# Performance work log

Hardware: AMD Instinct MI355X
Metric: run time of the kernel (lower is better)

Reference implementation:

```python
import jax, jax.numpy as jnp
import numpy as np
from jax import lax

DIM = 256
PROJ = 128
NPOS = 8          # ceil(log2(2*64+5))
EXT = 64          # attnExtension
NLAYERS = 4
HEADS = 4
KDIM = PROJ + NPOS
EPS = 1e-5


def _ln(x):
    # LayerNorm over last dim, no affine (elementwise_affine=False)
    mu = jnp.mean(x, axis=-1, keepdims=True)
    var = jnp.mean(jnp.square(x - mu), axis=-1, keepdims=True)
    return (x - mu) * lax.rsqrt(var + EPS)


def setup_inputs() -> dict:
    key = jax.random.key(0)
    ks = jax.random.split(key, 18)
    L = 2048
    s = 0.05
    return {
        "input": jax.random.normal(ks[0], (L, PROJ), jnp.float32),
        "residual": jax.random.normal(ks[1], (5 * L, DIM), jnp.float32),
        "W_proj": jax.random.normal(ks[2], (5 * DIM, KDIM), jnp.float32) * s,
        "b_proj": jnp.zeros((5 * DIM,), jnp.float32),
        "Wq": jax.random.normal(ks[3], (DIM, DIM), jnp.float32) * s,
        "bq": jnp.zeros((DIM,), jnp.float32),
        "Wk": jax.random.normal(ks[4], (DIM, KDIM), jnp.float32) * s,
        "bk": jnp.zeros((DIM,), jnp.float32),
        "Wv": jax.random.normal(ks[5], (DIM, KDIM), jnp.float32) * s,
        "bv": jnp.zeros((DIM,), jnp.float32),
        "Wo": jax.random.normal(ks[6], (DIM, DIM), jnp.float32) * s,
        "bo": jnp.zeros((DIM,), jnp.float32),
        "conv_w": jax.random.normal(ks[7], (NLAYERS, DIM, DIM, 3), jnp.float32) * s,
        "conv_b": jnp.zeros((NLAYERS, DIM), jnp.float32),
        "W_skip": jax.random.normal(ks[8], (DIM, DIM), jnp.float32) * s,
        "b_skip": jnp.zeros((DIM,), jnp.float32),
    }


def reference(input, residual, W_proj, b_proj, Wq, bq, Wk, bk, Wv, bv,
              Wo, bo, conv_w, conv_b, W_skip, b_skip):
    L = input.shape[0]
    T = 5 * L  # tgt length
    hd = DIM // HEADS

    # positional embeddings: pos[:, i] = (arange(L) % 2^(i+1)) / 2^i
    n = jnp.arange(L, dtype=input.dtype)[:, None]
    i = jnp.arange(NPOS, dtype=input.dtype)[None, :]
    pos = jnp.mod(n, 2.0 ** (i + 1.0)) / (2.0 ** i)

    src = jnp.concatenate([input, pos], axis=1)            # (L, KDIM)
    tgt = (src @ W_proj.T + b_proj).reshape(T, DIM)        # (5L, DIM)

    # banded mask: row j may attend col i iff 5i-EXT <= j < 5i+5+EXT
    j = jnp.arange(T)[:, None]
    ii = jnp.arange(L)[None, :]
    d = j - 5 * ii
    allowed = (d >= -EXT) & (d < 5 + EXT)                  # (5L, L)

    # multihead attention (eval mode, dropout skipped)
    q = (tgt @ Wq.T + bq).reshape(T, HEADS, hd).transpose(1, 0, 2)
    k = (src @ Wk.T + bk).reshape(L, HEADS, hd).transpose(1, 0, 2)
    v = (src @ Wv.T + bv).reshape(L, HEADS, hd).transpose(1, 0, 2)
    scores = jnp.einsum('hqd,hkd->hqk', q, k) / jnp.sqrt(jnp.asarray(hd, q.dtype))
    scores = jnp.where(allowed[None], scores, -jnp.inf)
    attn = jax.nn.softmax(scores, axis=-1)
    ctx = jnp.einsum('hqk,hkd->hqd', attn, v).transpose(1, 0, 2).reshape(T, DIM)
    attn_out = ctx @ Wo.T + bo

    cnn_in = _ln(attn_out) + residual                      # (5L, DIM)

    # spectral-norm conv stack (weights assumed pre-normalized) + tanh
    x = cnn_in.T[None]                                     # (1, DIM, 5L)
    for l in range(NLAYERS):
        x = jnp.tanh(
            lax.conv_general_dilated(x, conv_w[l], window_strides=(1,),
                                     padding=[(1, 1)])
            + conv_b[l][None, :, None])
    cnn_out = x[0].T                                       # (5L, DIM)

    return _ln(cnn_out + cnn_in @ W_skip.T + b_skip)
```

## Files before the change

### kernel.cpp

```cpp
#include <hip/hip_runtime.h>
#include <hip/hip_bf16.h>

#define PROJ 128
#define KPAD 192
#define EPS 1e-5f

typedef __attribute__((ext_vector_type(4))) float f32x4;
typedef __attribute__((ext_vector_type(8))) short bf16x8;
typedef __attribute__((ext_vector_type(4))) unsigned int u32x4;

__device__ inline float bflo(unsigned u){ union{unsigned x;float f;}c; c.x = u<<16; return c.f; }
__device__ inline float bfhi(unsigned u){ union{unsigned x;float f;}c; c.x = u & 0xffff0000u; return c.f; }
__device__ inline float bf2f(unsigned short u){ union{unsigned x;float f;}c; c.x = ((unsigned)u)<<16; return c.f; }
__device__ inline unsigned short f2bf(float f){
    union{float f; unsigned u;} c; c.f = f;
    unsigned r = c.u + 0x7fff + ((c.u >> 16) & 1);
    return (unsigned short)(r >> 16);
}

__global__ __launch_bounds__(256) void prep_all(
    const float* __restrict__ W_proj, const float* __restrict__ Wq,
    const float* __restrict__ Wk, const float* __restrict__ Wv,
    const float* __restrict__ Wo, const float* __restrict__ Ws,
    const float* __restrict__ convw, const float* __restrict__ input,
    unsigned short* __restrict__ Wpb, unsigned short* __restrict__ Wqb,
    unsigned short* __restrict__ Wkb, unsigned short* __restrict__ Wvb,
    unsigned short* __restrict__ Wob, unsigned short* __restrict__ Wsb,
    unsigned short* __restrict__ Wcb, unsigned short* __restrict__ srcb,
    unsigned short* __restrict__ cinp, int L, int T)
{
    int idx = blockIdx.x * 256 + threadIdx.x;
    if (idx < 245760) {
        int r = idx / 192, c = idx % 192;
        Wpb[idx] = (c < 136) ? f2bf(W_proj[(size_t)r * 136 + c]) : (unsigned short)0;
        return;
    }
    idx -= 245760;
    if (idx < 65536) { Wqb[idx] = f2bf(Wq[idx]); return; }
    idx -= 65536;
    if (idx < 49152) {
        int r = idx / 192, c = idx % 192;
        Wkb[idx] = (c < 136) ? f2bf(Wk[(size_t)r * 136 + c]) : (unsigned short)0;
        return;
    }
    idx -= 49152;
    if (idx < 49152) {
        int r = idx / 192, c = idx % 192;
        Wvb[idx] = (c < 136) ? f2bf(Wv[(size_t)r * 136 + c]) : (unsigned short)0;
        return;
    }
    idx -= 49152;
    if (idx < 65536) { Wob[idx] = f2bf(Wo[idx]); return; }
    idx -= 65536;
    if (idx < 65536) {
        int e = idx & 7;
        int lane = (idx >> 3) & 63;
        int fr = (idx >> 9) & 3;
        int wid = (idx >> 11) & 7;
        int kt = idx >> 14;
        int j = fr >> 1, ks = fr & 1;
        int kq = lane >> 4, rowf = lane & 15;
        int o = wid * 32 + j * 16 + rowf;
        int c = kt * 64 + ks * 32 + kq * 8 + e;
        Wsb[idx] = f2bf(Ws[(size_t)o * 256 + c]);
        return;
    }
    idx -= 65536;
    if (idx < 786432) {
        int e = idx & 7;
        int lane = (idx >> 3) & 63;
        int fr = (idx >> 9) & 3;
        int wid = (idx >> 11) & 7;
        int ktl = idx >> 14;
        int l = ktl / 12, kt = ktl % 12;
        int j = fr >> 1, ks = fr & 1;
        int kq = lane >> 4, rowf = lane & 15;
        int o = wid * 32 + j * 16 + rowf;
        int c = kt * 64 + ks * 32 + kq * 8 + e;
        int ktap = c >> 8, ci = c & 255;
        Wcb[idx] = f2bf(convw[(((size_t)l * 256 + o) * 256 + ci) * 3 + ktap]);
        return;
    }
    idx -= 786432;
    if (idx < L * KPAD) {
        int n = idx / KPAD, c = idx % KPAD;
        float v = 0.f;
        if (c < PROJ) v = input[(size_t)n * PROJ + c];
        else if (c < PROJ + 8) {
            int i = c - PROJ;
            int mask = (2 << i) - 1;
            v = (float)(n & mask) / (float)(1 << i);
        }
        srcb[idx] = f2bf(v);
        return;
    }
    idx -= L * KPAD;
    if (idx < 512) {
        int row = idx >> 8, c = idx & 255;
        size_t o = (row == 0) ? (size_t)c : (size_t)(T + 1) * 256 + c;
        cinp[o] = 0;
    }
}

__device__ __forceinline__ void gemm_core_64x128(
    unsigned short (&As)[64][72], unsigned short (&Bs)[128][72],
    const unsigned short* __restrict__ A, int lda,
    const unsigned short* __restrict__ B, int ldb,
    const float* __restrict__ bias,
    unsigned short* __restrict__ C, int ldc,
    int K, int m0, int n0)
{
    const int tid = threadIdx.x;
    const int lane = tid & 63;
    const int wid = tid >> 6;
    const int wm = wid >> 1, wn = wid & 1;

    const int ar = tid >> 2, asg = tid & 3;
    const int br = tid >> 1, bsg = tid & 1;

    const unsigned short* Ap = A + (size_t)(m0 + ar) * lda + asg * 16;
    const unsigned short* Bp = B + (size_t)(n0 + br) * ldb + bsg * 32;

    u32x4 ra0, ra1, rb0, rb1, rb2, rb3;
    auto loadregs = [&](int k0) {
        ra0 = *(const u32x4*)(Ap + k0);
        ra1 = *(const u32x4*)(Ap + k0 + 8);
        rb0 = *(const u32x4*)(Bp + k0);
        rb1 = *(const u32x4*)(Bp + k0 + 8);
        rb2 = *(const u32x4*)(Bp + k0 + 16);
        rb3 = *(const u32x4*)(Bp + k0 + 24);
    };
    auto stlds = [&]() {
        *(u32x4*)&As[ar][asg * 16]      = ra0;
        *(u32x4*)&As[ar][asg * 16 + 8]  = ra1;
        *(u32x4*)&Bs[br][bsg * 32]      = rb0;
        *(u32x4*)&Bs[br][bsg * 32 + 8]  = rb1;
        *(u32x4*)&Bs[br][bsg * 32 + 16] = rb2;
        *(u32x4*)&Bs[br][bsg * 32 + 24] = rb3;
    };

    f32x4 acc[2][4];
    #pragma unroll
    for (int i = 0; i < 2; ++i)
        #pragma unroll
        for (int j = 0; j < 4; ++j) acc[i][j] = (f32x4){0.f, 0.f, 0.f, 0.f};

    loadregs(0);
    stlds();
    __syncthreads();

    const int rowf = lane & 15, kb = lane >> 4;
    const int ktiles = K >> 6;
    for (int kt = 0; kt < ktiles; ++kt) {
        if (kt + 1 < ktiles) loadregs((kt + 1) << 6);
        #pragma unroll
        for (int ks = 0; ks < 2; ++ks) {
            bf16x8 af[2], bfr[4];
            #pragma unroll
            for (int i = 0; i < 2; ++i)
                af[i] = *(const bf16x8*)&As[wm * 32 + i * 16 + rowf][ks * 32 + kb * 8];
            #pragma unroll
            for (int j = 0; j < 4; ++j)
                bfr[j] = *(const bf16x8*)&Bs[wn * 64 + j * 16 + rowf][ks * 32 + kb * 8];
            #pragma unroll
            for (int i = 0; i < 2; ++i)
                #pragma unroll
                for (int j = 0; j < 4; ++j)
                    acc[i][j] = __builtin_amdgcn_mfma_f32_16x16x32_bf16(af[i], bfr[j], acc[i][j], 0, 0, 0);
        }
        __syncthreads();
        if (kt + 1 < ktiles) { stlds(); __syncthreads(); }
    }

    const int rq = lane >> 4;
    #pragma unroll
    for (int i = 0; i < 2; ++i) {
        int gm = m0 + wm * 32 + i * 16 + rq * 4;
        #pragma unroll
        for (int j = 0; j < 4; ++j) {
            int gn = n0 + wn * 64 + j * 16 + rowf;
            float bv = bias[gn];
            #pragma unroll
            for (int r = 0; r < 4; ++r)
                C[(size_t)(gm + r) * ldc + gn] = f2bf(acc[i][j][r] + bv);
        }
    }
}

__global__ __launch_bounds__(256) void gemm_proj(
    const unsigned short* __restrict__ A, int lda,
    const unsigned short* __restrict__ B, int ldb,
    const float* __restrict__ bias,
    unsigned short* __restrict__ C, int ldc, int K)
{
    __shared__ unsigned short As[64][72];
    __shared__ unsigned short Bs[128][72];
    gemm_core_64x128(As, Bs, A, lda, B, ldb, bias, C, ldc, K,
                     blockIdx.y * 64, blockIdx.x * 128);
}

__global__ __launch_bounds__(256) void qkv_fused(
    const unsigned short* __restrict__ tgt,
    const unsigned short* __restrict__ src,
    const unsigned short* __restrict__ Wqb,
    const unsigned short* __restrict__ Wkb,
    const unsigned short* __restrict__ Wvb,
    const float* __restrict__ bq, const float* __restrict__ bk,
    const float* __restrict__ bv,
    unsigned short* __restrict__ qb, unsigned short* __restrict__ kb,
    unsigned short* __restrict__ vb)
{
    __shared__ unsigned short As[64][72];
    __shared__ unsigned short Bs[128][72];
    int bi = blockIdx.x;
    const unsigned short *A, *B;
    const float* bias;
    unsigned short* C;
    int lda, ldb, K, m0, n0;
    if (bi < 320) {
        A = tgt; B = Wqb; bias = bq; C = qb; lda = 256; ldb = 256; K = 256;
        m0 = (bi >> 1) * 64; n0 = (bi & 1) * 128;
    } else if (bi < 384) {
        int t = bi - 320;
        A = src; B = Wkb; bias = bk; C = kb; lda = KPAD; ldb = 192; K = 192;
        m0 = (t >> 1) * 64; n0 = (t & 1) * 128;
    } else {
        int t = bi - 384;
        A = src; B = Wvb; bias = bv; C = vb; lda = KPAD; ldb = 192; K = 192;
        m0 = (t >> 1) * 64; n0 = (t & 1) * 128;
    }
    gemm_core_64x128(As, Bs, A, lda, B, ldb, bias, C, 256, K, m0, n0);
}

__global__ __launch_bounds__(512) void gemm_ln0(
    const unsigned short* __restrict__ A, int lda,
    const unsigned short* __restrict__ B,
    const float* __restrict__ bias,
    const float* __restrict__ residual,
    unsigned short* __restrict__ out_bf)
{
    __shared__ unsigned short As[64][72];
    __shared__ unsigned short Bs[256][72];
    __shared__ float redS[64][4];
    __shared__ float redQ[64][4];

    const int tid = threadIdx.x;
    const int lane = tid & 63;
    const int wid = tid >> 6;
    const int wm = wid >> 2, wn = wid & 3;
    const int m0 = blockIdx.x * 64;

    const int arow = tid >> 3, acol = (tid & 7) * 8;
    const int brow = tid >> 1, bcol = (tid & 1) * 32;
    const unsigned short* Ap = A + (size_t)(m0 + arow) * lda + acol;
    const unsigned short* Bp = B + (size_t)brow * 256 + bcol;

    u32x4 ra, rb0, rb1, rb2, rb3;
    auto loadregs = [&](int k0) {
        ra  = *(const u32x4*)(Ap + k0);
        rb0 = *(const u32x4*)(Bp + k0);
        rb1 = *(const u32x4*)(Bp + k0 + 8);
        rb2 = *(const u32x4*)(Bp + k0 + 16);
        rb3 = *(const u32x4*)(Bp + k0 + 24);
    };
    auto stlds = [&]() {
        *(u32x4*)&As[arow][acol]       = ra;
        *(u32x4*)&Bs[brow][bcol]       = rb0;
        *(u32x4*)&Bs[brow][bcol + 8]   = rb1;
        *(u32x4*)&Bs[brow][bcol + 16]  = rb2;
        *(u32x4*)&Bs[brow][bcol + 24]  = rb3;
    };

    f32x4 acc[2][4];
    #pragma unroll
    for (int i = 0; i < 2; ++i)
        #pragma unroll
        for (int j = 0; j < 4; ++j) acc[i][j] = (f32x4){0.f, 0.f, 0.f, 0.f};

    loadregs(0);
    stlds();
    __syncthreads();

    const int rowf = lane & 15, kb = lane >> 4;
    #pragma unroll
    for (int kt = 0; kt < 4; ++kt) {
        if (kt < 3) loadregs((kt + 1) << 6);
        #pragma unroll
        for (int ks = 0; ks < 2; ++ks) {
            bf16x8 af[2], bfr[4];
            #pragma unroll
            for (int i = 0; i < 2; ++i)
                af[i] = *(const bf16x8*)&As[wm * 32 + i * 16 + rowf][ks * 32 + kb * 8];
            #pragma unroll
            for (int j = 0; j < 4; ++j)
                bfr[j] = *(const bf16x8*)&Bs[wn * 64 + j * 16 + rowf][ks * 32 + kb * 8];
            #pragma unroll
            for (int i = 0; i < 2; ++i)
                #pragma unroll
                for (int j = 0; j < 4; ++j)
                    acc[i][j] = __builtin_amdgcn_mfma_f32_16x16x32_bf16(af[i], bfr[j], acc[i][j], 0, 0, 0);
        }
        __syncthreads();
        if (kt < 3) { stlds(); __syncthreads(); }
    }

    const int rq = lane >> 4;
    float val[2][4][4];
    #pragma unroll
    for (int i = 0; i < 2; ++i)
        #pragma unroll
        for (int j = 0; j < 4; ++j) {
            int gn = wn * 64 + j * 16 + rowf;
            float bv = bias[gn];
            #pragma unroll
            for (int r = 0; r < 4; ++r) val[i][j][r] = acc[i][j][r] + bv;
        }

    #pragma unroll
    for (int i = 0; i < 2; ++i)
        #pragma unroll
        for (int r = 0; r < 4; ++r) {
            float s = val[i][0][r] + val[i][1][r] + val[i][2][r] + val[i][3][r];
            float q = val[i][0][r] * val[i][0][r] + val[i][1][r] * val[i][1][r]
                    + val[i][2][r] * val[i][2][r] + val[i][3][r] * val[i][3][r];
            #pragma unroll
            for (int m = 1; m < 16; m <<= 1) {
                s += __shfl_xor(s, m, 64);
                q += __shfl_xor(q, m, 64);
            }
            if (rowf == 0) {
                int row = wm * 32 + i * 16 + rq * 4 + r;
                redS[row][wn] = s;
                redQ[row][wn] = q;
            }
        }
    __syncthreads();

    #pragma unroll
    for (int i = 0; i < 2; ++i) {
        #pragma unroll
        for (int r = 0; r < 4; ++r) {
            int row = wm * 32 + i * 16 + rq * 4 + r;
            int gm = m0 + row;
            float s = redS[row][0] + redS[row][1] + redS[row][2] + redS[row][3];
            float q = redQ[row][0] + redQ[row][1] + redQ[row][2] + redQ[row][3];
            float mu = s * (1.f / 256.f);
            float var = q * (1.f / 256.f) - mu * mu;
            float rs = rsqrtf(var + EPS);
            #pragma unroll
            for (int j = 0; j < 4; ++j) {
                int gn = wn * 64 + j * 16 + rowf;
                float nv = (val[i][j][r] - mu) * rs + residual[(size_t)gm * 256 + gn];
                out_bf[(size_t)(gm + 1) * 256 + gn] = f2bf(nv);
            }
        }
    }
}

__global__ __launch_bounds__(256) void attn16(
    const unsigned short* __restrict__ q,
    const unsigned short* __restrict__ k,
    const unsigned short* __restrict__ v,
    unsigned short* __restrict__ ctx, int L)
{
    __shared__ unsigned short ksm[30][264];
    __shared__ unsigned short vsm[30][264];
    const int j0 = blockIdx.x * 16;
    const int iblk0 = (j0 >= 68) ? (j0 - 64) / 5 : 0;
    int ihim = (j0 + 79) / 5; if (ihim > L - 1) ihim = L - 1;
    const int NR = ihim - iblk0 + 1;

    for (int e = threadIdx.x; e < 30 * 32; e += 256) {
        int rr = e >> 5, cc = (e & 31) * 8;
        u32x4 kz = {0, 0, 0, 0}, vz = {0, 0, 0, 0};
        if (rr < NR) {
            kz = *(const u32x4*)&k[(size_t)(iblk0 + rr) * 256 + cc];
            vz = *(const u32x4*)&v[(size_t)(iblk0 + rr) * 256 + cc];
        }
        *(u32x4*)&ksm[rr][cc] = kz;
        *(u32x4*)&vsm[rr][cc] = vz;
    }
    __syncthreads();

    const int tid = threadIdx.x;
    const int h = tid >> 6, lane = tid & 63;
    const int qq = lane & 15, p = lane >> 4;
    const int j = j0 + qq;
    const int colb = h * 64 + p * 16;

    float qr[16];
    {
        u32x4 q0 = *(const u32x4*)&q[(size_t)j * 256 + colb];
        u32x4 q1 = *(const u32x4*)&q[(size_t)j * 256 + colb + 8];
        #pragma unroll
        for (int w = 0; w < 4; ++w) {
            qr[2 * w]     = bflo(q0[w]) * 0.125f;
            qr[2 * w + 1] = bfhi(q0[w]) * 0.125f;
            qr[8 + 2 * w]     = bflo(q1[w]) * 0.125f;
            qr[8 + 2 * w + 1] = bfhi(q1[w]) * 0.125f;
        }
    }
    const int ilo = (j >= 68) ? (j - 64) / 5 : 0;
    int ihi = (j + 64) / 5; if (ihi > L - 1) ihi = L - 1;

    float sc[30];
    #pragma unroll
    for (int t = 0; t < 30; ++t) {
        int i = iblk0 + t;
        u32x4 k0 = *(const u32x4*)&ksm[t][colb];
        u32x4 k1 = *(const u32x4*)&ksm[t][colb + 8];
        float s = 0.f;
        #pragma unroll
        for (int w = 0; w < 4; ++w) {
            s += qr[2 * w]     * bflo(k0[w]);
            s += qr[2 * w + 1] * bfhi(k0[w]);
            s += qr[8 + 2 * w]     * bflo(k1[w]);
            s += qr[8 + 2 * w + 1] * bfhi(k1[w]);
        }
        s += __shfl_xor(s, 16, 64);
        s += __shfl_xor(s, 32, 64);
        sc[t] = (i >= ilo && i <= ihi) ? s : -1e30f;
    }
    float mx = -1e30f;
    #pragma unroll
    for (int t = 0; t < 30; ++t) mx = fmaxf(mx, sc[t]);
    float den = 0.f, o[16];
    #pragma unroll
    for (int d = 0; d < 16; ++d) o[d] = 0.f;
    #pragma unroll
    for (int t = 0; t < 30; ++t) {
        float pt = __expf(sc[t] - mx);
        den += pt;
        u32x4 v0 = *(const u32x4*)&vsm[t][colb];
        u32x4 v1 = *(const u32x4*)&vsm[t][colb + 8];
        #pragma unroll
        for (int w = 0; w < 4; ++w) {
            o[2 * w]     += pt * bflo(v0[w]);
            o[2 * w + 1] += pt * bfhi(v0[w]);
            o[8 + 2 * w]     += pt * bflo(v1[w]);
            o[8 + 2 * w + 1] += pt * bfhi(v1[w]);
        }
    }
    float inv = 1.f / den;
    #pragma unroll
    for (int d = 0; d < 16; ++d)
        ctx[(size_t)j * 256 + colb + d] = f2bf(o[d] * inv);
}

#define CVALID 40
template<int NKT, bool ISCONV>
__device__ __forceinline__ void frag_gemm(
    const unsigned short* __restrict__ Wp,
    unsigned short (*actin)[264],
    f32x4 (&acc)[3][2], int wid, int lane)
{
    const int rowf = lane & 15, kq = lane >> 4;
    const unsigned short* base = Wp + wid * 2048 + lane * 8;
    bf16x8 b0, b1, b2, b3, c0, c1, c2, c3, d0, d1, d2, d3;
    b0 = *(const bf16x8*)(base);
    b1 = *(const bf16x8*)(base + 512);
    b2 = *(const bf16x8*)(base + 1024);
    b3 = *(const bf16x8*)(base + 1536);
    c0 = *(const bf16x8*)(base + 16384);
    c1 = *(const bf16x8*)(base + 16384 + 512);
    c2 = *(const bf16x8*)(base + 16384 + 1024);
    c3 = *(const bf16x8*)(base + 16384 + 1536);
    d0 = b0; d1 = b1; d2 = b2; d3 = b3;
    #pragma unroll
    for (int kt = 0; kt < NKT; ++kt) {
        if (kt + 2 < NKT) {
            const unsigned short* nb = base + (kt + 2) * 16384;
            d0 = *(const bf16x8*)(nb);
            d1 = *(const bf16x8*)(nb + 512);
            d2 = *(const bf16x8*)(nb + 1024);
            d3 = *(const bf16x8*)(nb + 1536);
        }
        const int dt = ISCONV ? (kt >> 2) : 1;
        const int cb = ISCONV ? ((kt & 3) * 64) : (kt * 64);
        #pragma unroll
        for (int ks = 0; ks < 2; ++ks) {
            bf16x8 a0 = *(const bf16x8*)&actin[rowf + dt][cb + ks * 32 + kq * 8];
            bf16x8 a1 = *(const bf16x8*)&actin[16 + rowf + dt][cb + ks * 32 + kq * 8];
            bf16x8 a2 = *(const bf16x8*)&actin[32 + rowf + dt][cb + ks * 32 + kq * 8];
            bf16x8 w0 = ks ? b1 : b0;
            bf16x8 w1 = ks ? b3 : b2;
            acc[0][0] = __builtin_amdgcn_mfma_f32_16x16x32_bf16(a0, w0, acc[0][0], 0, 0, 0);
            acc[0][1] = __builtin_amdgcn_mfma_f32_16x16x32_bf16(a0, w1, acc[0][1], 0, 0, 0);
            acc[1][0] = __builtin_amdgcn_mfma_f32_16x16x32_bf16(a1, w0, acc[1][0], 0, 0, 0);
            acc[1][1] = __builtin_amdgcn_mfma_f32_16x16x32_bf16(a1, w1, acc[1][1], 0, 0, 0);
            acc[2][0] = __builtin_amdgcn_mfma_f32_16x16x32_bf16(a2, w0, acc[2][0], 0, 0, 0);
            acc[2][1] = __builtin_amdgcn_mfma_f32_16x16x32_bf16(a2, w1, acc[2][1], 0, 0, 0);
        }
        b0 = c0; b1 = c1; b2 = c2; b3 = c3;
        c0 = d0; c1 = d1; c2 = d2; c3 = d3;
    }
}

__global__ __launch_bounds__(512, 2) void conv_skip_ln(
    const unsigned short* __restrict__ cinp,
    const unsigned short* __restrict__ Wcb,
    const float* __restrict__ conv_b,
    const unsigned short* __restrict__ Wsb,
    const float* __restrict__ b_skip,
    float* __restrict__ out, int T)
{
    __shared__ unsigned short actA[50][264];
    __shared__ unsigned short actB[50][264];
    __shared__ float redS[48][8];
    __shared__ float redQ[48][8];

    const int tid = threadIdx.x;
    const int lane = tid & 63;
    const int wid = tid >> 6;
    const int rowf = lane & 15;
    const int kq = lane >> 4;
    const int t0 = blockIdx.x * CVALID;

    for (int e = tid; e < 50 * 32; e += 512) {
        int b = e >> 5, c = (e & 31) * 8;
        int g = t0 - 5 + b;
        u32x4 z = {0, 0, 0, 0};
        if (g >= -1 && g <= T)
            z = *(const u32x4*)&cinp[(size_t)(g + 1) * 256 + c];
        *(u32x4*)&actA[b][c] = z;
    }
    if (tid < 256) actB[0][tid] = 0; else actB[49][tid - 256] = 0;
    __syncthreads();

    f32x4 skipacc[3][2];
    #pragma unroll
    for (int i = 0; i < 3; ++i)
        #pragma unroll
        for (int j = 0; j < 2; ++j) skipacc[i][j] = (f32x4){0.f, 0.f, 0.f, 0.f};
    frag_gemm<4, false>(Wsb, actA, skipacc, wid, lane);

    const int gn0 = wid * 32 + rowf;
    f32x4 cacc[3][2];
    #pragma unroll 1
    for (int l = 0; l < 4; ++l) {
        #pragma unroll
        for (int i = 0; i < 3; ++i)
            #pragma unroll
            for (int j = 0; j < 2; ++j) cacc[i][j] = (f32x4){0.f, 0.f, 0.f, 0.f};
        unsigned short (*ain)[264]  = (l & 1) ? actB : actA;
        unsigned short (*aout)[264] = (l & 1) ? actA : actB;
        frag_gemm<12, true>(Wcb + (size_t)l * 196608, ain, cacc, wid, lane);

        float b0 = conv_b[l * 256 + gn0];
        float b1 = conv_b[l * 256 + gn0 + 16];
        if (l < 3) {
            #pragma unroll
            for (int i = 0; i < 3; ++i)
                #pragma unroll
                for (int r = 0; r < 4; ++r) {
                    int w = i * 16 + kq * 4 + r;
                    int g = t0 - 4 + w;
                    bool ok = (g >= 0 && g < T);
                    float v0 = cacc[i][0][r] + b0;
                    float v1 = cacc[i][1][r] + b1;
                    v0 = 1.f - 2.f / (__expf(2.f * v0) + 1.f);
                    v1 = 1.f - 2.f / (__expf(2.f * v1) + 1.f);
                    aout[w + 1][gn0]      = ok ? f2bf(v0) : (unsigned short)0;
                    aout[w + 1][gn0 + 16] = ok ? f2bf(v1) : (unsigned short)0;
                }
            if (tid < 256) aout[0][tid] = 0; else aout[49][tid - 256] = 0;
            __syncthreads();
        } else {
            float sb0 = b_skip[gn0], sb1 = b_skip[gn0 + 16];
            #pragma unroll
            for (int i = 0; i < 3; ++i)
                #pragma unroll
                for (int r = 0; r < 4; ++r) {
                    int w = i * 16 + kq * 4 + r;
                    int g = t0 - 4 + w;
                    bool ok = (g >= 0 && g < T);
                    float v0 = cacc[i][0][r] + b0;
                    float v1 = cacc[i][1][r] + b1;
                    v0 = ok ? (1.f - 2.f / (__expf(2.f * v0) + 1.f)) : 0.f;
                    v1 = ok ? (1.f - 2.f / (__expf(2.f * v1) + 1.f)) : 0.f;
                    skipacc[i][0][r] += sb0 + v0;
                    skipacc[i][1][r] += sb1 + v1;
                }
        }
    }

    #pragma unroll
    for (int i = 0; i < 3; ++i)
        #pragma unroll
        for (int r = 0; r < 4; ++r) {
            float a = skipacc[i][0][r], b = skipacc[i][1][r];
            float s = a + b;
            float q = a * a + b * b;
            #pragma unroll
            for (int m = 1; m < 16; m <<= 1) {
                s += __shfl_xor(s, m, 64);
                q += __shfl_xor(q, m, 64);
            }
            if (rowf == 0) {
                int row = i * 16 + kq * 4 + r;
                redS[row][wid] = s;
                redQ[row][wid] = q;
            }
        }
    __syncthreads();

    #pragma unroll
    for (int i = 0; i < 3; ++i)
        #pragma unroll
        for (int r = 0; r < 4; ++r) {
            int row = i * 16 + kq * 4 + r;
            if (row < 4 || row >= 44) continue;
            int g = t0 - 4 + row;
            if (g >= T) continue;
            float s = 0.f, q = 0.f;
            #pragma unroll
            for (int x = 0; x < 8; ++x) { s += redS[row][x]; q += redQ[row][x]; }
            float mu = s * (1.f / 256.f);
            float var = q * (1.f / 256.f) - mu * mu;
            float rs = rsqrtf(var + EPS);
            out[(size_t)g * 256 + gn0]      = (skipacc[i][0][r] - mu) * rs;
            out[(size_t)g * 256 + gn0 + 16] = (skipacc[i][1][r] - mu) * rs;
        }
}

extern "C" void kernel_launch(void* const* d_in, const int* in_sizes, int n_in,
                              void* d_out, int out_size, void* d_ws, size_t ws_size,
                              hipStream_t stream) {
    const float* input    = (const float*)d_in[0];
    const float* residual = (const float*)d_in[1];
    const float* W_proj   = (const float*)d_in[2];
    const float* b_proj   = (const float*)d_in[3];
    const float* Wq       = (const float*)d_in[4];
    const float* bq       = (const float*)d_in[5];
    const float* Wk       = (const float*)d_in[6];
    const float* bk       = (const float*)d_in[7];
    const float* Wv       = (const float*)d_in[8];
    const float* bv       = (const float*)d_in[9];
    const float* Wo       = (const float*)d_in[10];
    const float* bo       = (const float*)d_in[11];
    const float* conv_w   = (const float*)d_in[12];
    const float* conv_b   = (const float*)d_in[13];
    const float* W_skip   = (const float*)d_in[14];
    const float* b_skip   = (const float*)d_in[15];
    float* out = (float*)d_out;

    const int L = in_sizes[0] / PROJ;
    const int T = 5 * L;

    unsigned short* w16 = (unsigned short*)d_ws;
    size_t off = 0;
    auto alloc = [&](size_t n) { unsigned short* p = w16 + off; off += n; return p; };
    unsigned short* Wpb  = alloc((size_t)1280 * 192);
    unsigned short* Wqb  = alloc(256 * 256);
    unsigned short* Wkb  = alloc(256 * 192);
    unsigned short* Wvb  = alloc(256 * 192);
    unsigned short* Wob  = alloc(256 * 256);
    unsigned short* Wsb  = alloc(256 * 256);
    unsigned short* Wcb  = alloc((size_t)4 * 256 * 768);
    unsigned short* srcb = alloc((size_t)L * KPAD);
    unsigned short* tgtb = alloc((size_t)T * 256);
    unsigned short* qb   = alloc((size_t)T * 256);
    unsigned short* kb   = alloc((size_t)L * 256);
    unsigned short* vb   = alloc((size_t)L * 256);
    unsigned short* cinp = alloc((size_t)(T + 2) * 256);

    prep_all<<<dim3(6722), 256, 0, stream>>>(
        W_proj, Wq, Wk, Wv, Wo, W_skip, conv_w, input,
        Wpb, Wqb, Wkb, Wvb, Wob, Wsb, Wcb, srcb, cinp, L, T);

    gemm_proj<<<dim3(1280 / 128, L / 64), 256, 0, stream>>>(
        srcb, KPAD, Wpb, 192, b_proj, tgtb, 1280, 192);

    qkv_fused<<<dim3(448), 256, 0, stream>>>(
        tgtb, srcb, Wqb, Wkb, Wvb, bq, bk, bv, qb, kb, vb);

    attn16<<<dim3(T / 16), 256, 0, stream>>>(qb, kb, vb, tgtb, L);

    gemm_ln0<<<dim3(T / 64), 512, 0, stream>>>(tgtb, 256, Wob, bo, residual, cinp);

    conv_skip_ln<<<dim3(T / CVALID), 512, 0, stream>>>(
        cinp, Wcb, conv_b, Wsb, b_skip, out, T);
}
```

Measured before the change: 93.55 us.

## Fold input projection into Wq to compute Q directly from src

Precomputes combined weights Wq·W_proj per projection chunk (a small GEMM) and the matching folded bias, so Q is produced directly from src with K=192 instead of first materializing tgt and then multiplying by Wq. This removes the separate projection GEMM and the tgt round trip before the Q GEMM. The conv weight prefetch depth is also cut from two tiles to one, and the conv kernel's launch bounds change from 2 to 1 blocks per SM minimum. Risks: the extra bf16 rounding of the combined weights changes numerics, and tgtb is still passed to attention as its output buffer.

```diff
diff --git a/kernel.cpp b/kernel.cpp
--- a/kernel.cpp
+++ b/kernel.cpp
@@ -23,19 +23,15 @@
     const float* __restrict__ Wk, const float* __restrict__ Wv,
     const float* __restrict__ Wo, const float* __restrict__ Ws,
     const float* __restrict__ convw, const float* __restrict__ input,
-    unsigned short* __restrict__ Wpb, unsigned short* __restrict__ Wqb,
-    unsigned short* __restrict__ Wkb, unsigned short* __restrict__ Wvb,
-    unsigned short* __restrict__ Wob, unsigned short* __restrict__ Wsb,
-    unsigned short* __restrict__ Wcb, unsigned short* __restrict__ srcb,
-    unsigned short* __restrict__ cinp, int L, int T)
+    const float* __restrict__ bq, const float* __restrict__ b_proj,
+    unsigned short* __restrict__ Wqb, unsigned short* __restrict__ Wkb,
+    unsigned short* __restrict__ Wvb, unsigned short* __restrict__ Wob,
+    unsigned short* __restrict__ Wsb, unsigned short* __restrict__ Wcb,
+    unsigned short* __restrict__ WpbT, unsigned short* __restrict__ srcb,
+    unsigned short* __restrict__ cinp, float* __restrict__ zbias,
+    float* __restrict__ bqc, int L, int T)
 {
     int idx = blockIdx.x * 256 + threadIdx.x;
-    if (idx < 245760) {
-        int r = idx / 192, c = idx % 192;
-        Wpb[idx] = (c < 136) ? f2bf(W_proj[(size_t)r * 136 + c]) : (unsigned short)0;
-        return;
-    }
-    idx -= 245760;
     if (idx < 65536) { Wqb[idx] = f2bf(Wq[idx]); return; }
     idx -= 65536;
     if (idx < 49152) {
@@ -82,6 +78,15 @@
         return;
     }
     idx -= 786432;
+    if (idx < 327680) {
+        int r = idx >> 16;
+        int rem = idx & 65535;
+        int c = rem >> 8, d = rem & 255;
+        WpbT[idx] = (c < 136) ? f2bf(W_proj[(size_t)(r * 256 + d) * 136 + c])
+                              : (unsigned short)0;
+        return;
+    }
+    idx -= 327680;
     if (idx < L * KPAD) {
         int n = idx / KPAD, c = idx % KPAD;
         float v = 0.f;
@@ -99,6 +104,18 @@
         int row = idx >> 8, c = idx & 255;
         size_t o = (row == 0) ? (size_t)c : (size_t)(T + 1) * 256 + c;
         cinp[o] = 0;
+        return;
+    }
+    idx -= 512;
+    if (idx < 256) { zbias[idx] = 0.f; return; }
+    idx -= 256;
+    if (idx < 1280) {
+        int r = idx >> 8, o = idx & 255;
+        float s = bq[o];
+        const float* wrow = Wq + (size_t)o * 256;
+        const float* bp = b_proj + r * 256;
+        for (int c = 0; c < 256; ++c) s += wrow[c] * bp[c];
+        bqc[idx] = s;
     }
 }
 
@@ -187,25 +204,27 @@
     }
 }
 
-__global__ __launch_bounds__(256) void gemm_proj(
-    const unsigned short* __restrict__ A, int lda,
-    const unsigned short* __restrict__ B, int ldb,
-    const float* __restrict__ bias,
-    unsigned short* __restrict__ C, int ldc, int K)
+__global__ __launch_bounds__(256) void combine_wq(
+    const unsigned short* __restrict__ Wqb,
+    const unsigned short* __restrict__ WpbT,
+    const float* __restrict__ zbias,
+    unsigned short* __restrict__ Wqpb)
 {
     __shared__ unsigned short As[64][72];
     __shared__ unsigned short Bs[128][72];
-    gemm_core_64x128(As, Bs, A, lda, B, ldb, bias, C, ldc, K,
-                     blockIdx.y * 64, blockIdx.x * 128);
+    int bi = blockIdx.x;
+    int r = bi >> 3, rem = bi & 7;
+    int m0 = (rem >> 1) * 64, n0 = (rem & 1) * 128;
+    gemm_core_64x128(As, Bs, Wqb, 256, WpbT + (size_t)r * 65536, 256, zbias,
+                     Wqpb + (size_t)r * 65536, 256, 256, m0, n0);
 }
 
 __global__ __launch_bounds__(256) void qkv_fused(
-    const unsigned short* __restrict__ tgt,
-    const unsigned short* __restrict__ src,
-    const unsigned short* __restrict__ Wqb,
+    const unsigned short* __restrict__ srcb,
+    const unsigned short* __restrict__ Wqpb,
     const unsigned short* __restrict__ Wkb,
     const unsigned short* __restrict__ Wvb,
-    const float* __restrict__ bq, const float* __restrict__ bk,
+    const float* __restrict__ bqc, const float* __restrict__ bk,
     const float* __restrict__ bv,
     unsigned short* __restrict__ qb, unsigned short* __restrict__ kb,
     unsigned short* __restrict__ vb)
@@ -213,23 +232,23 @@
     __shared__ unsigned short As[64][72];
     __shared__ unsigned short Bs[128][72];
     int bi = blockIdx.x;
-    const unsigned short *A, *B;
+    const unsigned short *B;
     const float* bias;
     unsigned short* C;
-    int lda, ldb, K, m0, n0;
+    int ldb, K, m0, n0, ldc;
     if (bi < 320) {
-        A = tgt; B = Wqb; bias = bq; C = qb; lda = 256; ldb = 256; K = 256;
-        m0 = (bi >> 1) * 64; n0 = (bi & 1) * 128;
+        B = Wqpb; bias = bqc; C = qb; ldb = 256; K = 192; ldc = 1280;
+        m0 = (bi / 10) * 64; n0 = (bi % 10) * 128;
     } else if (bi < 384) {
         int t = bi - 320;
-        A = src; B = Wkb; bias = bk; C = kb; lda = KPAD; ldb = 192; K = 192;
+        B = Wkb; bias = bk; C = kb; ldb = 192; K = 192; ldc = 256;
         m0 = (t >> 1) * 64; n0 = (t & 1) * 128;
     } else {
         int t = bi - 384;
-        A = src; B = Wvb; bias = bv; C = vb; lda = KPAD; ldb = 192; K = 192;
+        B = Wvb; bias = bv; C = vb; ldb = 192; K = 192; ldc = 256;
         m0 = (t >> 1) * 64; n0 = (t & 1) * 128;
     }
-    gemm_core_64x128(As, Bs, A, lda, B, ldb, bias, C, 256, K, m0, n0);
+    gemm_core_64x128(As, Bs, srcb, KPAD, B, ldb, bias, C, ldc, K, m0, n0);
 }
 
 __global__ __launch_bounds__(512) void gemm_ln0(
@@ -456,24 +475,19 @@
 {
     const int rowf = lane & 15, kq = lane >> 4;
     const unsigned short* base = Wp + wid * 2048 + lane * 8;
-    bf16x8 b0, b1, b2, b3, c0, c1, c2, c3, d0, d1, d2, d3;
-    b0 = *(const bf16x8*)(base);
-    b1 = *(const bf16x8*)(base + 512);
-    b2 = *(const bf16x8*)(base + 1024);
-    b3 = *(const bf16x8*)(base + 1536);
-    c0 = *(const bf16x8*)(base + 16384);
-    c1 = *(const bf16x8*)(base + 16384 + 512);
-    c2 = *(const bf16x8*)(base + 16384 + 1024);
-    c3 = *(const bf16x8*)(base + 16384 + 1536);
-    d0 = b0; d1 = b1; d2 = b2; d3 = b3;
+    bf16x8 cur0, cur1, cur2, cur3, nxt0, nxt1, nxt2, nxt3;
+    cur0 = *(const bf16x8*)(base);
+    cur1 = *(const bf16x8*)(base + 512);
+    cur2 = *(const bf16x8*)(base + 1024);
+    cur3 = *(const bf16x8*)(base + 1536);
     #pragma unroll
     for (int kt = 0; kt < NKT; ++kt) {
-        if (kt + 2 < NKT) {
-            const unsigned short* nb = base + (kt + 2) * 16384;
-            d0 = *(const bf16x8*)(nb);
-            d1 = *(const bf16x8*)(nb + 512);
-            d2 = *(const bf16x8*)(nb + 1024);
-            d3 = *(const bf16x8*)(nb + 1536);
+        if (kt + 1 < NKT) {
+            const unsigned short* nb = base + (kt + 1) * 16384;
+            nxt0 = *(const bf16x8*)(nb);
+            nxt1 = *(const bf16x8*)(nb + 512);
+            nxt2 = *(const bf16x8*)(nb + 1024);
+            nxt3 = *(const bf16x8*)(nb + 1536);
         }
         const int dt = ISCONV ? (kt >> 2) : 1;
         const int cb = ISCONV ? ((kt & 3) * 64) : (kt * 64);
@@ -482,8 +496,8 @@
             bf16x8 a0 = *(const bf16x8*)&actin[rowf + dt][cb + ks * 32 + kq * 8];
             bf16x8 a1 = *(const bf16x8*)&actin[16 + rowf + dt][cb + ks * 32 + kq * 8];
             bf16x8 a2 = *(const bf16x8*)&actin[32 + rowf + dt][cb + ks * 32 + kq * 8];
-            bf16x8 w0 = ks ? b1 : b0;
-            bf16x8 w1 = ks ? b3 : b2;
+            bf16x8 w0 = ks ? cur1 : cur0;
+            bf16x8 w1 = ks ? cur3 : cur2;
             acc[0][0] = __builtin_amdgcn_mfma_f32_16x16x32_bf16(a0, w0, acc[0][0], 0, 0, 0);
             acc[0][1] = __builtin_amdgcn_mfma_f32_16x16x32_bf16(a0, w1, acc[0][1], 0, 0, 0);
             acc[1][0] = __builtin_amdgcn_mfma_f32_16x16x32_bf16(a1, w0, acc[1][0], 0, 0, 0);
@@ -491,12 +505,11 @@
             acc[2][0] = __builtin_amdgcn_mfma_f32_16x16x32_bf16(a2, w0, acc[2][0], 0, 0, 0);
             acc[2][1] = __builtin_amdgcn_mfma_f32_16x16x32_bf16(a2, w1, acc[2][1], 0, 0, 0);
         }
-        b0 = c0; b1 = c1; b2 = c2; b3 = c3;
-        c0 = d0; c1 = d1; c2 = d2; c3 = d3;
-    }
-}
-
-__global__ __launch_bounds__(512, 2) void conv_skip_ln(
+        cur0 = nxt0; cur1 = nxt1; cur2 = nxt2; cur3 = nxt3;
+    }
+}
+
+__global__ __launch_bounds__(512, 1) void conv_skip_ln(
     const unsigned short* __restrict__ cinp,
     const unsigned short* __restrict__ Wcb,
     const float* __restrict__ conv_b,
@@ -650,29 +663,31 @@
     unsigned short* w16 = (unsigned short*)d_ws;
     size_t off = 0;
     auto alloc = [&](size_t n) { unsigned short* p = w16 + off; off += n; return p; };
-    unsigned short* Wpb  = alloc((size_t)1280 * 192);
-    unsigned short* Wqb  = alloc(256 * 256);
-    unsigned short* Wkb  = alloc(256 * 192);
-    unsigned short* Wvb  = alloc(256 * 192);
-    unsigned short* Wob  = alloc(256 * 256);
-    unsigned short* Wsb  = alloc(256 * 256);
-    unsigned short* Wcb  = alloc((size_t)4 * 256 * 768);
-    unsigned short* srcb = alloc((size_t)L * KPAD);
-    unsigned short* tgtb = alloc((size_t)T * 256);
-    unsigned short* qb   = alloc((size_t)T * 256);
-    unsigned short* kb   = alloc((size_t)L * 256);
-    unsigned short* vb   = alloc((size_t)L * 256);
-    unsigned short* cinp = alloc((size_t)(T + 2) * 256);
-
-    prep_all<<<dim3(6722), 256, 0, stream>>>(
-        W_proj, Wq, Wk, Wv, Wo, W_skip, conv_w, input,
-        Wpb, Wqb, Wkb, Wvb, Wob, Wsb, Wcb, srcb, cinp, L, T);
-
-    gemm_proj<<<dim3(1280 / 128, L / 64), 256, 0, stream>>>(
-        srcb, KPAD, Wpb, 192, b_proj, tgtb, 1280, 192);
+    unsigned short* Wqb   = alloc(65536);
+    unsigned short* Wkb   = alloc(49152);
+    unsigned short* Wvb   = alloc(49152);
+    unsigned short* Wob   = alloc(65536);
+    unsigned short* Wsb   = alloc(65536);
+    unsigned short* Wcb   = alloc(786432);
+    unsigned short* WpbT  = alloc(327680);
+    unsigned short* Wqpb  = alloc(327680);
+    unsigned short* srcb  = alloc((size_t)L * KPAD);
+    unsigned short* tgtb  = alloc((size_t)T * 256);
+    unsigned short* qb    = alloc((size_t)T * 256);
+    unsigned short* kb    = alloc((size_t)L * 256);
+    unsigned short* vb    = alloc((size_t)L * 256);
+    unsigned short* cinp  = alloc((size_t)(T + 2) * 256);
+    float* zbias = (float*)alloc(512);
+    float* bqc   = (float*)alloc(2560);
+
+    prep_all<<<dim3(7048), 256, 0, stream>>>(
+        W_proj, Wq, Wk, Wv, Wo, W_skip, conv_w, input, bq, b_proj,
+        Wqb, Wkb, Wvb, Wob, Wsb, Wcb, WpbT, srcb, cinp, zbias, bqc, L, T);
+
+    combine_wq<<<dim3(40), 256, 0, stream>>>(Wqb, WpbT, zbias, Wqpb);
 
     qkv_fused<<<dim3(448), 256, 0, stream>>>(
-        tgtb, srcb, Wqb, Wkb, Wvb, bq, bk, bv, qb, kb, vb);
+        srcb, Wqpb, Wkb, Wvb, bqc, bk, bv, qb, kb, vb);
 
     attn16<<<dim3(T / 16), 256, 0, stream>>>(qb, kb, vb, tgtb, L);
 
```

Measured after the change: 99.47 us. +6.3%, slower.
